# Kernel tuning notes

Hardware: AMD Instinct MI355X
Metric: run time of the kernel (lower is better)

## Reference

```python
import jax, jax.numpy as jnp
import numpy as np

EMB_DIM = 1024
NUM_HEAD = 16
HEAD_DIM = EMB_DIM // NUM_HEAD
B, S = 2, 2048


def setup_inputs() -> dict:
    key = jax.random.key(0)
    ks = jax.random.split(key, 10)
    scale = 1.0 / np.sqrt(EMB_DIM)
    x = jax.random.normal(ks[0], (B, S, EMB_DIM), dtype=jnp.float32)
    # causal mask: 1 = keep, 0 = masked out (torch masked_fill(mask == 0, -inf))
    mask = jnp.tril(jnp.ones((S, S), dtype=jnp.int32))[None, None, :, :]
    def lin(kw, kb):
        W = jax.random.uniform(kw, (EMB_DIM, EMB_DIM), jnp.float32, -scale, scale)
        b = jax.random.uniform(kb, (EMB_DIM,), jnp.float32, -scale, scale)
        return W, b
    Wq, bq = lin(ks[1], ks[2])
    Wk, bk = lin(ks[3], ks[4])
    Wv, bv = lin(ks[5], ks[6])
    Wo, bo = lin(ks[7], ks[8])
    return {"x": x, "mask": mask, "Wq": Wq, "bq": bq, "Wk": Wk, "bk": bk,
            "Wv": Wv, "bv": bv, "Wo": Wo, "bo": bo}


def reference(x, mask, Wq, bq, Wk, bk, Wv, bv, Wo, bo):
    Bsz, Sq, _ = x.shape
    # projections; torch Linear: y = x @ W^T + b
    def proj(W, b):
        y = jnp.einsum('bse,fe->bsf', x, W) + b
        return y.reshape(Bsz, Sq, NUM_HEAD, HEAD_DIM).transpose(0, 2, 1, 3)  # [B,H,S,D]
    q = proj(Wq, bq)
    k = proj(Wk, bk)
    v = proj(Wv, bv)
    scaling = jnp.asarray(HEAD_DIM ** 0.5, x.dtype)
    scores = jnp.einsum('bhqd,bhkd->bhqk', q, k) / scaling  # [B,H,S,S]
    scores = jnp.where(mask == 0, -jnp.inf, scores)
    attn = jax.nn.softmax(scores, axis=-1)
    out = jnp.einsum('bhqk,bhkd->bhqd', attn, v)
    out = out.transpose(0, 2, 1, 3).reshape(Bsz, Sq, EMB_DIM)
    return jnp.einsum('bse,fe->bsf', out, Wo) + bo
```

## Files before the change

### kernel.cpp

```cpp
#include <hip/hip_runtime.h>

typedef unsigned short u16;
typedef __attribute__((ext_vector_type(8))) __bf16 bf16x8;
typedef __attribute__((ext_vector_type(8))) short  short8;
typedef __attribute__((ext_vector_type(4))) short  short4v;
typedef __attribute__((ext_vector_type(4))) float  floatx4;
typedef __attribute__((ext_vector_type(4))) int    intx4;

constexpr int Bc = 2, Sc = 2048, Ec = 1024, Hc = 16, Dc = 64;
constexpr int Mc = Bc * Sc;

#define QSCALE  0.18033688011112042f

__device__ __forceinline__ u16 f2b(float f) {
  union { float f; unsigned u; } c; c.f = f;
  unsigned u = c.u;
  return (u16)((u + 0x7fffu + ((u >> 16) & 1u)) >> 16);
}
__device__ __forceinline__ short8 ld8(const u16* p) { return *(const short8*)p; }

__device__ __forceinline__ int cvt_pk(float lo, float hi) {
  int r;
  asm("v_cvt_pk_bf16_f32 %0, %1, %2" : "=v"(r) : "v"(lo), "v"(hi));
  return r;
}

__device__ __forceinline__ floatx4 mfma16(short8 a, short8 b, floatx4 c) {
  return __builtin_amdgcn_mfma_f32_16x16x32_bf16(
      __builtin_bit_cast(bf16x8, a), __builtin_bit_cast(bf16x8, b), c, 0, 0, 0);
}

__device__ __forceinline__ void async16(const u16* g, u16* l) {
  __builtin_amdgcn_global_load_lds(
      (const __attribute__((address_space(1))) void*)g,
      (__attribute__((address_space(3))) void*)l, 16, 0, 0);
}

__global__ __launch_bounds__(256) void cvt_kernel(
    const float* __restrict__ x,  const float* __restrict__ Wq,
    const float* __restrict__ Wk, const float* __restrict__ Wv,
    const float* __restrict__ Wo, u16* __restrict__ dst) {
  const size_t i = ((size_t)blockIdx.x * 256 + threadIdx.x) * 4;
  const int seg = (int)(i >> 20);
  const float* src;
  size_t off;
  if (seg < 4)       { src = x;  off = i; }
  else if (seg == 4) { src = Wq; off = i - ((size_t)4 << 20); }
  else if (seg == 5) { src = Wk; off = i - ((size_t)5 << 20); }
  else if (seg == 6) { src = Wv; off = i - ((size_t)6 << 20); }
  else               { src = Wo; off = i - ((size_t)7 << 20); }
  floatx4 v = *(const floatx4*)(src + off);
  short4v o;
  o[0] = (short)f2b(v[0]); o[1] = (short)f2b(v[1]);
  o[2] = (short)f2b(v[2]); o[3] = (short)f2b(v[3]);
  *(short4v*)(dst + i) = o;
}

__device__ __forceinline__ void gemm128(
    const u16* __restrict__ A, const u16* __restrict__ B, int K,
    int m0, int n0, u16* As, u16* Bs, floatx4 acc[4][4]) {
  const int t = threadIdx.x;
  const int w = t >> 6, lane = t & 63;
  const int wm = w & 1, wn = w >> 1;
  const int quad = lane >> 4, l16 = lane & 15;
  const int r = t >> 2;
  const int c = (t & 3) * 8;

#pragma unroll
  for (int i = 0; i < 4; ++i)
#pragma unroll
    for (int j = 0; j < 4; ++j) acc[i][j] = 0.f;

  for (int k0 = 0; k0 < K; k0 += 32) {
#pragma unroll
    for (int jj = 0; jj < 2; ++jj) {
      async16(A + (size_t)(m0 + jj * 64 + r) * K + k0 + c, As + jj * 2048 + w * 512);
      async16(B + (size_t)(n0 + jj * 64 + r) * K + k0 + c, Bs + jj * 2048 + w * 512);
    }
    __syncthreads();
    short8 af[4], bfr[4];
#pragma unroll
    for (int i = 0; i < 4; ++i)
      af[i]  = *(const short8*)(As + (wm * 64 + i * 16 + l16) * 32 + quad * 8);
#pragma unroll
    for (int j = 0; j < 4; ++j)
      bfr[j] = *(const short8*)(Bs + (wn * 64 + j * 16 + l16) * 32 + quad * 8);
#pragma unroll
    for (int i = 0; i < 4; ++i)
#pragma unroll
      for (int j = 0; j < 4; ++j)
        acc[i][j] = mfma16(af[i], bfr[j], acc[i][j]);
    __syncthreads();
  }
}

__global__ __launch_bounds__(256) void qkv_mm(
    const u16* __restrict__ xb, const u16* __restrict__ Wb,
    const float* __restrict__ bq, const float* __restrict__ bk,
    const float* __restrict__ bv,
    u16* __restrict__ Q, u16* __restrict__ K_, u16* __restrict__ Vt) {
  __shared__ __align__(16) u16 As[4096], Bs[4096];
  const int z = blockIdx.z;
  const u16* W = Wb + ((size_t)z << 20);
  const float* bias = (z == 0) ? bq : (z == 1) ? bk : bv;
  const int m0 = blockIdx.y * 128, n0 = blockIdx.x * 128;

  floatx4 acc[4][4];
  gemm128(xb, W, Ec, m0, n0, As, Bs, acc);

  const int t = threadIdx.x, w = t >> 6, lane = t & 63;
  const int wm = w & 1, wn = w >> 1, quad = lane >> 4, l16 = lane & 15;
#pragma unroll
  for (int i = 0; i < 4; ++i)
#pragma unroll
    for (int j = 0; j < 4; ++j)
#pragma unroll
      for (int rr = 0; rr < 4; ++rr) {
        const int row = m0 + wm * 64 + i * 16 + quad * 4 + rr;
        const int col = n0 + wn * 64 + j * 16 + l16;
        float v = acc[i][j][rr] + bias[col];
        if (z == 0) v *= QSCALE;
        const int bb = row >> 11, s = row & (Sc - 1);
        const int h = col >> 6, d = col & (Dc - 1), bh = bb * Hc + h;
        if (z < 2) ((z == 0) ? Q : K_)[((size_t)bh * Sc + s) * Dc + d] = f2b(v);
        else {
          const int sp = (s & ~31) | ((s & 12) << 1) | ((s & 16) >> 2) | (s & 3);
          Vt[((size_t)bh * Dc + d) * Sc + sp] = f2b(v);
        }
      }
}

__global__ __launch_bounds__(256) void proj_mm(
    const u16* __restrict__ O, const u16* __restrict__ Wob,
    const float* __restrict__ bias, float* __restrict__ out) {
  __shared__ __align__(16) u16 As[4096], Bs[4096];
  const int m0 = blockIdx.y * 128, n0 = blockIdx.x * 128;

  floatx4 acc[4][4];
  gemm128(O, Wob, Ec, m0, n0, As, Bs, acc);

  const int t = threadIdx.x, w = t >> 6, lane = t & 63;
  const int wm = w & 1, wn = w >> 1, quad = lane >> 4, l16 = lane & 15;
#pragma unroll
  for (int i = 0; i < 4; ++i)
#pragma unroll
    for (int j = 0; j < 4; ++j)
#pragma unroll
      for (int rr = 0; rr < 4; ++rr) {
        const int row = m0 + wm * 64 + i * 16 + quad * 4 + rr;
        const int col = n0 + wn * 64 + j * 16 + l16;
        out[(size_t)row * Ec + col] = acc[i][j][rr] + bias[col];
      }
}

__global__ __launch_bounds__(256, 4) void attn_kernel(
    const u16* __restrict__ Q, const u16* __restrict__ K,
    const u16* __restrict__ Vt, u16* __restrict__ O) {
  const int v  = blockIdx.x & 31, g8 = blockIdx.x >> 5, kk = blockIdx.y;
  const int q1 = (kk & 2) ? ((v + 8) & 31) : v;
  const int qt = (kk & 1) ? (31 - q1) : q1;
  const int q0 = qt * 64;
  const int bh = kk * 8 + g8;
  const int bb = bh >> 4, h = bh & 15;

  const u16* Qh = Q  + (size_t)bh * Sc * Dc;
  const u16* Kh = K  + (size_t)bh * Sc * Dc;
  const u16* Vh = Vt + (size_t)bh * Dc * Sc;

  const int t = threadIdx.x;
  const int w = t >> 6, lane = t & 63;
  const int quad = lane >> 4, l16 = lane & 15;

  __shared__ __align__(16) u16 Ks[8192];
  __shared__ __align__(16) u16 Vs[8192];

  const int sr = w * 8 + (lane >> 3);
  const int sb = (lane & 7) ^ (lane >> 3);
  const int swz = l16 & 7;

  const u16* qrow_p = Qh + (size_t)(q0 + w * 16 + l16) * Dc;
  const short8 aq0 = ld8(qrow_p + quad * 8);
  const short8 aq1 = ld8(qrow_p + 32 + quad * 8);

  float   lrow = 0.f;
  floatx4 oacc[4];
#pragma unroll
  for (int dt = 0; dt < 4; ++dt) oacc[dt] = 0.f;

  for (int kt = 0; kt <= q0; kt += 128) {
#pragma unroll
    for (int st = 0; st < 2; ++st)
#pragma unroll
      for (int it = 0; it < 2; ++it) {
        const int r = it * 32 + sr;
        async16(Kh + (size_t)(kt + st * 64 + r) * Dc + sb * 8,
                Ks + st * 4096 + it * 2048 + w * 512);
        async16(Vh + (size_t)r * Sc + kt + st * 64 + sb * 8,
                Vs + st * 4096 + it * 2048 + w * 512);
      }
    __syncthreads();

    floatx4 sacc[8];
#pragma unroll
    for (int g = 0; g < 8; ++g) sacc[g] = 0.f;
#pragma unroll
    for (int ks = 0; ks < 2; ++ks) {
      const short8 bq = ks ? aq1 : aq0;
#pragma unroll
      for (int g = 0; g < 8; ++g) {
        const short8 a = *(const short8*)(
            Ks + (g >> 2) * 4096 + ((g & 3) * 16 + l16) * 64 +
            (((ks * 4 + quad) ^ swz) * 8));
        sacc[g] = mfma16(a, bq, sacc[g]);
      }
    }

    const bool diag = (kt + 128 > q0);
    const int thr = q0 + w * 16 + l16 - kt - 4 * quad;
#pragma unroll
    for (int g = 0; g < 8; ++g)
#pragma unroll
      for (int r = 0; r < 4; ++r) {
        float pv = exp2f(sacc[g][r]);
        if (diag && (16 * g + r > thr)) pv = 0.f;
        lrow += pv;
        sacc[g][r] = pv;
      }

    short8 pa[4];
#pragma unroll
    for (int c = 0; c < 4; ++c) {
      intx4 wd;
      wd[0] = cvt_pk(sacc[2 * c][0],     sacc[2 * c][1]);
      wd[1] = cvt_pk(sacc[2 * c][2],     sacc[2 * c][3]);
      wd[2] = cvt_pk(sacc[2 * c + 1][0], sacc[2 * c + 1][1]);
      wd[3] = cvt_pk(sacc[2 * c + 1][2], sacc[2 * c + 1][3]);
      pa[c] = __builtin_bit_cast(short8, wd);
    }

#pragma unroll
    for (int c = 0; c < 4; ++c) {
      const int st = c >> 1, kcl = c & 1;
#pragma unroll
      for (int dt = 0; dt < 4; ++dt) {
        const short8 b = *(const short8*)(
            Vs + st * 4096 + (dt * 16 + l16) * 64 +
            (((kcl * 4 + quad) ^ swz) * 8));
        oacc[dt] = mfma16(pa[c], b, oacc[dt]);
      }
    }
    __syncthreads();
  }

  lrow += __shfl_xor(lrow, 16);
  lrow += __shfl_xor(lrow, 32);
  float rs[4];
#pragma unroll
  for (int r = 0; r < 4; ++r)
    rs[r] = 1.f / __shfl(lrow, quad * 4 + r, 16);

#pragma unroll
  for (int dt = 0; dt < 4; ++dt) {
#pragma unroll
    for (int r = 0; r < 4; ++r) {
      const int qrow = q0 + w * 16 + quad * 4 + r;
      O[((size_t)(bb * Sc + qrow)) * Ec + h * Dc + dt * 16 + l16] =
          f2b(oacc[dt][r] * rs[r]);
    }
  }
}

extern "C" void kernel_launch(void* const* d_in, const int* in_sizes, int n_in,
                              void* d_out, int out_size, void* d_ws, size_t ws_size,
                              hipStream_t stream) {
  const float* x  = (const float*)d_in[0];
  const float* Wq = (const float*)d_in[2];
  const float* bq = (const float*)d_in[3];
  const float* Wk = (const float*)d_in[4];
  const float* bk = (const float*)d_in[5];
  const float* Wv = (const float*)d_in[6];
  const float* bv = (const float*)d_in[7];
  const float* Wo = (const float*)d_in[8];
  const float* bo = (const float*)d_in[9];

  const size_t MiE = (size_t)Mc * Ec;
  u16* Q  = (u16*)d_ws;
  u16* K  = Q  + MiE;
  u16* Vt = K  + MiE;
  u16* O  = Vt + MiE;
  u16* xb = O  + MiE;
  u16* Wb = xb + MiE;
  u16* Wob = Wb + ((size_t)3 << 20);

  cvt_kernel<<<8192, 256, 0, stream>>>(x, Wq, Wk, Wv, Wo, xb);
  qkv_mm<<<dim3(Ec / 128, Mc / 128, 3), 256, 0, stream>>>(
      xb, Wb, bq, bk, bv, Q, K, Vt);
  attn_kernel<<<dim3(256, 4), 256, 0, stream>>>(Q, K, Vt, O);
  proj_mm<<<dim3(Ec / 128, Mc / 128), 256, 0, stream>>>(O, Wob, bo, (float*)d_out);
}
```

Before: 202.0 us.

## Double-buffer GEMM LDS tiles, swizzle LDS layout, stage V-transpose store through LDS

```diff
diff --git a/kernel.cpp b/kernel.cpp
--- a/kernel.cpp
+++ b/kernel.cpp
@@ -64,33 +64,49 @@
   const int wm = w & 1, wn = w >> 1;
   const int quad = lane >> 4, l16 = lane & 15;
   const int r = t >> 2;
-  const int c = (t & 3) * 8;
+  const int c = ((t & 3) ^ ((t >> 3) & 3)) * 8;
+  const int rsw = (l16 >> 1) & 3;
 
 #pragma unroll
   for (int i = 0; i < 4; ++i)
 #pragma unroll
     for (int j = 0; j < 4; ++j) acc[i][j] = 0.f;
 
+#pragma unroll
+  for (int jj = 0; jj < 2; ++jj) {
+    async16(A + (size_t)(m0 + jj * 64 + r) * K + c, As + jj * 2048 + w * 512);
+    async16(B + (size_t)(n0 + jj * 64 + r) * K + c, Bs + jj * 2048 + w * 512);
+  }
+  __syncthreads();
+
+  int cur = 0;
   for (int k0 = 0; k0 < K; k0 += 32) {
-#pragma unroll
-    for (int jj = 0; jj < 2; ++jj) {
-      async16(A + (size_t)(m0 + jj * 64 + r) * K + k0 + c, As + jj * 2048 + w * 512);
-      async16(B + (size_t)(n0 + jj * 64 + r) * K + k0 + c, Bs + jj * 2048 + w * 512);
-    }
-    __syncthreads();
+    const int nxt = cur ^ 1;
+    if (k0 + 32 < K) {
+#pragma unroll
+      for (int jj = 0; jj < 2; ++jj) {
+        async16(A + (size_t)(m0 + jj * 64 + r) * K + (k0 + 32) + c,
+                As + nxt * 4096 + jj * 2048 + w * 512);
+        async16(B + (size_t)(n0 + jj * 64 + r) * K + (k0 + 32) + c,
+                Bs + nxt * 4096 + jj * 2048 + w * 512);
+      }
+    }
     short8 af[4], bfr[4];
 #pragma unroll
     for (int i = 0; i < 4; ++i)
-      af[i]  = *(const short8*)(As + (wm * 64 + i * 16 + l16) * 32 + quad * 8);
+      af[i]  = *(const short8*)(As + cur * 4096 +
+                (wm * 64 + i * 16 + l16) * 32 + (quad ^ rsw) * 8);
 #pragma unroll
     for (int j = 0; j < 4; ++j)
-      bfr[j] = *(const short8*)(Bs + (wn * 64 + j * 16 + l16) * 32 + quad * 8);
+      bfr[j] = *(const short8*)(Bs + cur * 4096 +
+                (wn * 64 + j * 16 + l16) * 32 + (quad ^ rsw) * 8);
 #pragma unroll
     for (int i = 0; i < 4; ++i)
 #pragma unroll
       for (int j = 0; j < 4; ++j)
         acc[i][j] = mfma16(af[i], bfr[j], acc[i][j]);
     __syncthreads();
+    cur = nxt;
   }
 }
 
@@ -99,7 +115,7 @@
     const float* __restrict__ bq, const float* __restrict__ bk,
     const float* __restrict__ bv,
     u16* __restrict__ Q, u16* __restrict__ K_, u16* __restrict__ Vt) {
-  __shared__ __align__(16) u16 As[4096], Bs[4096];
+  __shared__ __align__(16) u16 As[8192], Bs[8192];
   const int z = blockIdx.z;
   const u16* W = Wb + ((size_t)z << 20);
   const float* bias = (z == 0) ? bq : (z == 1) ? bk : bv;
@@ -110,30 +126,64 @@
 
   const int t = threadIdx.x, w = t >> 6, lane = t & 63;
   const int wm = w & 1, wn = w >> 1, quad = lane >> 4, l16 = lane & 15;
-#pragma unroll
-  for (int i = 0; i < 4; ++i)
-#pragma unroll
-    for (int j = 0; j < 4; ++j)
-#pragma unroll
-      for (int rr = 0; rr < 4; ++rr) {
-        const int row = m0 + wm * 64 + i * 16 + quad * 4 + rr;
-        const int col = n0 + wn * 64 + j * 16 + l16;
-        float v = acc[i][j][rr] + bias[col];
-        if (z == 0) v *= QSCALE;
-        const int bb = row >> 11, s = row & (Sc - 1);
+
+  if (z < 2) {
+#pragma unroll
+    for (int i = 0; i < 4; ++i)
+#pragma unroll
+      for (int j = 0; j < 4; ++j)
+#pragma unroll
+        for (int rr = 0; rr < 4; ++rr) {
+          const int row = m0 + wm * 64 + i * 16 + quad * 4 + rr;
+          const int col = n0 + wn * 64 + j * 16 + l16;
+          float v = acc[i][j][rr] + bias[col];
+          if (z == 0) v *= QSCALE;
+          const int bb = row >> 11, s = row & (Sc - 1);
+          const int h = col >> 6, d = col & (Dc - 1), bh = bb * Hc + h;
+          ((z == 0) ? Q : K_)[((size_t)bh * Sc + s) * Dc + d] = f2b(v);
+        }
+  } else {
+    u16* Tb = wn ? Bs : As;
+#pragma unroll
+    for (int j = 0; j < 4; ++j) {
+      const int col_local = j * 16 + l16;
+      const float bcol = bias[n0 + wn * 64 + col_local];
+#pragma unroll
+      for (int i = 0; i < 4; ++i) {
+        const int blk  = wm * 8 + (i & 2) * 2 + quad;
+        const int blks = (blk & 8) | ((blk & 7) ^ (col_local & 7));
+        short4v o;
+        o[0] = (short)f2b(acc[i][j][0] + bcol);
+        o[1] = (short)f2b(acc[i][j][1] + bcol);
+        o[2] = (short)f2b(acc[i][j][2] + bcol);
+        o[3] = (short)f2b(acc[i][j][3] + bcol);
+        *(short4v*)(Tb + col_local * 128 + blks * 8 + (i & 1) * 4) = o;
+      }
+    }
+    __syncthreads();
+    const int bb = m0 >> 11;
+    const int s0 = m0 & (Sc - 1);
+#pragma unroll
+    for (int bi = 0; bi < 2; ++bi) {
+      const u16* Tr = bi ? Bs : As;
+#pragma unroll
+      for (int cc = 0; cc < 4; ++cc) {
+        const int cid = cc * 256 + t;
+        const int dl = cid >> 4, sc = cid & 15;
+        const int scs = (sc & 8) | ((sc & 7) ^ (dl & 7));
+        const int col = n0 + bi * 64 + dl;
         const int h = col >> 6, d = col & (Dc - 1), bh = bb * Hc + h;
-        if (z < 2) ((z == 0) ? Q : K_)[((size_t)bh * Sc + s) * Dc + d] = f2b(v);
-        else {
-          const int sp = (s & ~31) | ((s & 12) << 1) | ((s & 16) >> 2) | (s & 3);
-          Vt[((size_t)bh * Dc + d) * Sc + sp] = f2b(v);
-        }
-      }
+        *(short8*)(Vt + ((size_t)bh * Dc + d) * Sc + s0 + sc * 8) =
+            *(const short8*)(Tr + dl * 128 + scs * 8);
+      }
+    }
+  }
 }
 
 __global__ __launch_bounds__(256) void proj_mm(
     const u16* __restrict__ O, const u16* __restrict__ Wob,
     const float* __restrict__ bias, float* __restrict__ out) {
-  __shared__ __align__(16) u16 As[4096], Bs[4096];
+  __shared__ __align__(16) u16 As[8192], Bs[8192];
   const int m0 = blockIdx.y * 128, n0 = blockIdx.x * 128;
 
   floatx4 acc[4][4];
```

Result: slower. 214.3 us (+6.1%).
